# Optimization experiments

Measured on AMD Instinct MI355X. Metric: run time of the kernel, lower is better.

Reference implementation:

```python
import jax, jax.numpy as jnp
import numpy as np

K = 3          # k_neighbors
EPS = 1e-12    # F.normalize eps


def _l2norm(x):
    n = jnp.sqrt(jnp.sum(x * x, axis=-1, keepdims=True))
    return x / jnp.maximum(n, EPS)


def setup_inputs() -> dict:
    key = jax.random.key(0)
    k1, k2 = jax.random.split(key)
    query_features = jax.random.normal(k1, (64, 64, 32, 32), dtype=jnp.float32)
    support_features = jax.random.normal(k2, (64, 5, 64, 1024), dtype=jnp.float32)
    return {"query_features": query_features, "support_features": support_features}


def reference(query_features, support_features):
    B, D, h, w = query_features.shape
    # (B, Nq, D), L2-normalized along D
    q_local = _l2norm(query_features.reshape(B, D, h * w).transpose(0, 2, 1))
    # support: (B, Way, D, Ns) -> (B, Way, Ns, D), L2-normalized along D
    s_local = _l2norm(support_features.transpose(0, 1, 3, 2))
    # cosine similarities for all (batch, way) pairs in one batched matmul
    sim = jnp.einsum('bqd,bwsd->bwqs', q_local, s_local)  # (B, Way, Nq, Ns)
    k_actual = min(K, sim.shape[-1])
    topk_sim, _ = jax.lax.top_k(sim, k_actual)            # (B, Way, Nq, k)
    return topk_sim.sum(axis=(-1, -2))                    # (B, Way)
```

## Files before the change

kernel.cpp:

```cpp
#include <hip/hip_runtime.h>
#include <hip/hip_bf16.h>


using bf16x8 = __attribute__((ext_vector_type(8))) short;
using f32x4  = __attribute__((ext_vector_type(4))) float;

__device__ inline unsigned cvt_pk_bf16(float lo, float hi) {
    unsigned r;
    asm("v_cvt_pk_bf16_f32 %0, %1, %2" : "=v"(r) : "v"(lo), "v"(hi));
    return r;
}

__device__ inline uint4 pack8cvt(const float* v) {
    uint4 r;
    r.x = cvt_pk_bf16(v[0], v[1]);
    r.y = cvt_pk_bf16(v[2], v[3]);
    r.z = cvt_pk_bf16(v[4], v[5]);
    r.w = cvt_pk_bf16(v[6], v[7]);
    return r;
}

#define INS(v, T0, T1, T2) do {                         \
    float _v = (v);                                     \
    float _n0 = fmaxf((T0), _v);                        \
    float _n1 = __builtin_amdgcn_fmed3f(_v, (T0), (T1));\
    float _n2 = __builtin_amdgcn_fmed3f(_v, (T1), (T2));\
    (T0) = _n0; (T1) = _n1; (T2) = _n2;                 \
} while (0)

__global__ void norms_kernel(const float* __restrict__ Q, const float* __restrict__ S,
                             float* __restrict__ rnq, float* __restrict__ rns) {
    int gid = blockIdx.x * blockDim.x + threadIdx.x;
    if (gid < 65536) {
        int b = gid >> 10, qi = gid & 1023;
        const float* p = Q + (size_t)b * 65536 + qi;
        float ss = 0.f;
        #pragma unroll
        for (int d = 0; d < 64; ++d) { float v = p[(size_t)d * 1024]; ss += v * v; }
        rnq[gid] = 1.0f / fmaxf(sqrtf(ss), 1e-12f);
    } else {
        int v = gid - 65536;
        int bw = v >> 10, si = v & 1023;
        const float* p = S + (size_t)bw * 65536 + si;
        float ss = 0.f;
        #pragma unroll
        for (int d = 0; d < 64; ++d) { float x = p[(size_t)d * 1024]; ss += x * x; }
        rns[v] = 1.0f / fmaxf(sqrtf(ss), 1e-12f);
    }
}

__global__ __launch_bounds__(512, 4) void knn_main(
        const float* __restrict__ Q, const float* __restrict__ S,
        const float* __restrict__ rnq, const float* __restrict__ rns,
        float* __restrict__ partial) {
    __shared__ uint4 qfrag[16 * 128];
    __shared__ uint4 sfrag[2][4 * 128];
    __shared__ float wsum[8];

    const int qc = blockIdx.x, w = blockIdx.y, b = blockIdx.z;
    const int t = threadIdx.x, wv = t >> 6, lane = t & 63;

    const float* Qb   = Q + (size_t)b * 65536;
    const float* Sb   = S + (size_t)(b * 5 + w) * 65536;
    const float* rnqb = rnq + (b << 10);
    const float* rnsb = rns + ((b * 5 + w) << 10);

    bf16x8 bq[4][2];
    for (int ph = 0; ph < 2; ++ph) {
        for (int sub = 0; sub < 4; ++sub) {
            int qg = (qc << 9) + (ph << 8) + (sub << 6) + lane;
            float v[8];
            #pragma unroll
            for (int i = 0; i < 8; ++i)
                v[i] = Qb[(size_t)((wv << 3) + i) * 1024 + qg];
            qfrag[((sub << 2) + (lane >> 4)) * 128 + (wv << 4) + (lane & 15)] = pack8cvt(v);
        }
        __syncthreads();
        if ((wv >> 2) == ph) {
            #pragma unroll
            for (int qt = 0; qt < 4; ++qt)
                #pragma unroll
                for (int c = 0; c < 2; ++c)
                    bq[qt][c] = *reinterpret_cast<const bf16x8*>(
                        &qfrag[(((wv & 3) << 2) + qt) * 128 + (c << 6) + lane]);
        }
        __syncthreads();
    }

    {
        float sv[8]; float rs = rnsb[lane];
        #pragma unroll
        for (int i = 0; i < 8; ++i)
            sv[i] = Sb[(size_t)((wv << 3) + i) * 1024 + lane] * rs;
        sfrag[0][(lane >> 4) * 128 + (wv << 4) + (lane & 15)] = pack8cvt(sv);
    }
    __syncthreads();

    float t0[4], t1[4], t2[4];
    #pragma unroll
    for (int qt = 0; qt < 4; ++qt) { t0[qt] = -1e30f; t1[qt] = -1e30f; t2[qt] = -1e30f; }
    int cur = 0;

    const float* sp = Sb + ((wv << 3) << 10) + lane;

    for (int blk = 0; blk < 16; ++blk) {
        float sv[8]; float rs;
        if (blk < 15) {
            const int sb = (blk + 1) << 6;
            rs = rnsb[sb + lane];
            #pragma unroll
            for (int i = 0; i < 8; ++i)
                sv[i] = sp[(size_t)(i << 10) + sb];
        }
        #pragma unroll
        for (int st = 0; st < 4; ++st) {
            bf16x8 a0 = *reinterpret_cast<const bf16x8*>(&sfrag[cur][st * 128 + lane]);
            bf16x8 a1 = *reinterpret_cast<const bf16x8*>(&sfrag[cur][st * 128 + 64 + lane]);
            #pragma unroll
            for (int qt = 0; qt < 4; ++qt) {
                f32x4 c = {0.f, 0.f, 0.f, 0.f};
                c = __builtin_amdgcn_mfma_f32_16x16x32_bf16(a0, bq[qt][0], c, 0, 0, 0);
                c = __builtin_amdgcn_mfma_f32_16x16x32_bf16(a1, bq[qt][1], c, 0, 0, 0);
                #pragma unroll
                for (int j = 0; j < 4; ++j)
                    INS(c[j], t0[qt], t1[qt], t2[qt]);
            }
        }
        if (blk < 15) {
            #pragma unroll
            for (int i = 0; i < 8; ++i) sv[i] *= rs;
            sfrag[cur ^ 1][(lane >> 4) * 128 + (wv << 4) + (lane & 15)] = pack8cvt(sv);
        }
        __syncthreads();
        cur ^= 1;
    }

    float s3 = 0.f;
    #pragma unroll
    for (int qt = 0; qt < 4; ++qt) {
        #pragma unroll
        for (int m = 16; m <= 32; m <<= 1) {
            float b0 = __shfl_xor(t0[qt], m);
            float b1 = __shfl_xor(t1[qt], m);
            float b2 = __shfl_xor(t2[qt], m);
            INS(b0, t0[qt], t1[qt], t2[qt]);
            INS(b1, t0[qt], t1[qt], t2[qt]);
            INS(b2, t0[qt], t1[qt], t2[qt]);
        }
        int qg = (qc << 9) + (wv << 6) + (qt << 4) + (lane & 15);
        s3 += (t0[qt] + t1[qt] + t2[qt]) * rnqb[qg];
    }
    #pragma unroll
    for (int m = 1; m < 64; m <<= 1) s3 += __shfl_xor(s3, m);
    s3 *= 0.25f;
    if (lane == 0) wsum[wv] = s3;
    __syncthreads();
    if (t == 0) {
        float acc = 0.f;
        #pragma unroll
        for (int i = 0; i < 8; ++i) acc += wsum[i];
        partial[((b * 5 + w) << 1) + qc] = acc;
    }
}

__global__ void finalize_kernel(const float* __restrict__ partial, float* __restrict__ out) {
    int i = blockIdx.x * blockDim.x + threadIdx.x;
    if (i < 320)
        out[i] = partial[2 * i] + partial[2 * i + 1];
}

extern "C" void kernel_launch(void* const* d_in, const int* in_sizes, int n_in,
                              void* d_out, int out_size, void* d_ws, size_t ws_size,
                              hipStream_t stream) {
    const float* Q = (const float*)d_in[0];
    const float* S = (const float*)d_in[1];
    float* out = (float*)d_out;

    float* rnq = (float*)d_ws;
    float* rns = rnq + 65536;
    float* partial = rns + 327680;

    norms_kernel<<<(65536 + 327680) / 256, 256, 0, stream>>>(Q, S, rnq, rns);
    dim3 grid(2, 5, 64);
    knn_main<<<grid, 512, 0, stream>>>(Q, S, rnq, rns, partial);
    finalize_kernel<<<2, 256, 0, stream>>>(partial, out);
}
```

Before: 100.0 us.

## Pre-convert Q and S to bf16 MFMA-fragment layout in workspace before KNN

```diff
diff --git a/kernel.cpp b/kernel.cpp
--- a/kernel.cpp
+++ b/kernel.cpp
@@ -28,6 +28,119 @@
     (T0) = _n0; (T1) = _n1; (T2) = _n2;                 \
 } while (0)
 
+
+__global__ __launch_bounds__(256) void prep_q(const float* __restrict__ Q,
+                                              uint4* __restrict__ Qbf,
+                                              float* __restrict__ rnq) {
+    const int b = blockIdx.x >> 2;
+    const int col = ((blockIdx.x & 3) << 8) + threadIdx.x;
+    const float* p = Q + (size_t)b * 65536 + col;
+    float v[64];
+    #pragma unroll
+    for (int d = 0; d < 64; ++d) v[d] = p[(size_t)d << 10];
+    float ss = 0.f;
+    #pragma unroll
+    for (int d = 0; d < 64; ++d) ss += v[d] * v[d];
+    rnq[(b << 10) + col] = 1.0f / fmaxf(sqrtf(ss), 1e-12f);
+    uint4* ob = Qbf + ((size_t)(b << 6) + (col >> 4)) * 128 + (col & 15);
+    #pragma unroll
+    for (int h = 0; h < 8; ++h)
+        ob[h << 4] = pack8cvt(&v[h << 3]);
+}
+
+__global__ __launch_bounds__(256) void prep_s(const float* __restrict__ S,
+                                              uint4* __restrict__ Sbf) {
+    const int bw = blockIdx.x >> 2;
+    const int col = ((blockIdx.x & 3) << 8) + threadIdx.x;
+    const float* p = S + (size_t)bw * 65536 + col;
+    float v[64];
+    #pragma unroll
+    for (int d = 0; d < 64; ++d) v[d] = p[(size_t)d << 10];
+    float ss = 0.f;
+    #pragma unroll
+    for (int d = 0; d < 64; ++d) ss += v[d] * v[d];
+    const float rs = 1.0f / fmaxf(sqrtf(ss), 1e-12f);
+    #pragma unroll
+    for (int d = 0; d < 64; ++d) v[d] *= rs;
+    uint4* ob = Sbf + ((size_t)(bw << 6) + (col >> 4)) * 128 + (col & 15);
+    #pragma unroll
+    for (int h = 0; h < 8; ++h)
+        ob[h << 4] = pack8cvt(&v[h << 3]);
+}
+
+__global__ __launch_bounds__(256) void knn_main(const uint4* __restrict__ Qbf,
+                                                const uint4* __restrict__ Sbf,
+                                                const float* __restrict__ rnq,
+                                                float* __restrict__ partial) {
+    __shared__ float wsum[4];
+    const int qc = blockIdx.x, w = blockIdx.y, b = blockIdx.z;
+    const int wv = threadIdx.x >> 6, lane = threadIdx.x & 63;
+
+    const uint4* qb = Qbf + ((size_t)(b << 6) + (qc << 4) + (wv << 2)) * 128 + lane;
+    bf16x8 bq[4][2];
+    #pragma unroll
+    for (int qt = 0; qt < 4; ++qt)
+        #pragma unroll
+        for (int c = 0; c < 2; ++c)
+            bq[qt][c] = *reinterpret_cast<const bf16x8*>(&qb[qt * 128 + (c << 6)]);
+
+    const uint4* sb = Sbf + (size_t)((b * 5 + w) << 6) * 128 + lane;
+
+    float t0[4], t1[4], t2[4];
+    #pragma unroll
+    for (int qt = 0; qt < 4; ++qt) { t0[qt] = -1e30f; t1[qt] = -1e30f; t2[qt] = -1e30f; }
+
+    bf16x8 a0 = *reinterpret_cast<const bf16x8*>(&sb[0]);
+    bf16x8 a1 = *reinterpret_cast<const bf16x8*>(&sb[64]);
+    #pragma unroll 4
+    for (int st = 0; st < 64; ++st) {
+        const bf16x8 c0 = a0, c1 = a1;
+        if (st < 63) {
+            a0 = *reinterpret_cast<const bf16x8*>(&sb[(st + 1) * 128]);
+            a1 = *reinterpret_cast<const bf16x8*>(&sb[(st + 1) * 128 + 64]);
+        }
+        #pragma unroll
+        for (int qt = 0; qt < 4; ++qt) {
+            f32x4 c = {0.f, 0.f, 0.f, 0.f};
+            c = __builtin_amdgcn_mfma_f32_16x16x32_bf16(c0, bq[qt][0], c, 0, 0, 0);
+            c = __builtin_amdgcn_mfma_f32_16x16x32_bf16(c1, bq[qt][1], c, 0, 0, 0);
+            #pragma unroll
+            for (int j = 0; j < 4; ++j)
+                INS(c[j], t0[qt], t1[qt], t2[qt]);
+        }
+    }
+
+    float s3 = 0.f;
+    #pragma unroll
+    for (int qt = 0; qt < 4; ++qt) {
+        #pragma unroll
+        for (int m = 16; m <= 32; m <<= 1) {
+            float b0 = __shfl_xor(t0[qt], m);
+            float b1 = __shfl_xor(t1[qt], m);
+            float b2 = __shfl_xor(t2[qt], m);
+            INS(b0, t0[qt], t1[qt], t2[qt]);
+            INS(b1, t0[qt], t1[qt], t2[qt]);
+            INS(b2, t0[qt], t1[qt], t2[qt]);
+        }
+        const int qg = (qc << 8) + (wv << 6) + (qt << 4) + (lane & 15);
+        s3 += (t0[qt] + t1[qt] + t2[qt]) * rnq[(b << 10) + qg];
+    }
+    #pragma unroll
+    for (int m = 1; m < 64; m <<= 1) s3 += __shfl_xor(s3, m);
+    s3 *= 0.25f;
+    if (lane == 0) wsum[wv] = s3;
+    __syncthreads();
+    if (threadIdx.x == 0)
+        partial[((b * 5 + w) << 2) + qc] = (wsum[0] + wsum[1]) + (wsum[2] + wsum[3]);
+}
+
+__global__ void finalize4(const float* __restrict__ partial, float* __restrict__ out) {
+    int i = blockIdx.x * blockDim.x + threadIdx.x;
+    if (i < 320)
+        out[i] = (partial[4 * i] + partial[4 * i + 1]) +
+                 (partial[4 * i + 2] + partial[4 * i + 3]);
+}
+
 __global__ void norms_kernel(const float* __restrict__ Q, const float* __restrict__ S,
                              float* __restrict__ rnq, float* __restrict__ rns) {
     int gid = blockIdx.x * blockDim.x + threadIdx.x;
@@ -49,7 +162,7 @@
     }
 }
 
-__global__ __launch_bounds__(512, 4) void knn_main(
+__global__ __launch_bounds__(512, 4) void knn_fb(
         const float* __restrict__ Q, const float* __restrict__ S,
         const float* __restrict__ rnq, const float* __restrict__ rns,
         float* __restrict__ partial) {
@@ -100,17 +213,16 @@
     #pragma unroll
     for (int qt = 0; qt < 4; ++qt) { t0[qt] = -1e30f; t1[qt] = -1e30f; t2[qt] = -1e30f; }
     int cur = 0;
-
     const float* sp = Sb + ((wv << 3) << 10) + lane;
 
     for (int blk = 0; blk < 16; ++blk) {
         float sv[8]; float rs;
         if (blk < 15) {
-            const int sb = (blk + 1) << 6;
-            rs = rnsb[sb + lane];
+            const int sb_ = (blk + 1) << 6;
+            rs = rnsb[sb_ + lane];
             #pragma unroll
             for (int i = 0; i < 8; ++i)
-                sv[i] = sp[(size_t)(i << 10) + sb];
+                sv[i] = sp[(size_t)(i << 10) + sb_];
         }
         #pragma unroll
         for (int st = 0; st < 4; ++st) {
@@ -163,7 +275,7 @@
     }
 }
 
-__global__ void finalize_kernel(const float* __restrict__ partial, float* __restrict__ out) {
+__global__ void finalize2(const float* __restrict__ partial, float* __restrict__ out) {
     int i = blockIdx.x * blockDim.x + threadIdx.x;
     if (i < 320)
         out[i] = partial[2 * i] + partial[2 * i + 1];
@@ -176,12 +288,22 @@
     const float* S = (const float*)d_in[1];
     float* out = (float*)d_out;
 
-    float* rnq = (float*)d_ws;
-    float* rns = rnq + 65536;
-    float* partial = rns + 327680;
-
-    norms_kernel<<<(65536 + 327680) / 256, 256, 0, stream>>>(Q, S, rnq, rns);
-    dim3 grid(2, 5, 64);
-    knn_main<<<grid, 512, 0, stream>>>(Q, S, rnq, rns, partial);
-    finalize_kernel<<<2, 256, 0, stream>>>(partial, out);
-}
+    const size_t NEED = 8388608ull + 41943040ull + 262144ull + 5120ull;
+    if (ws_size >= NEED) {
+        uint4* Qbf    = (uint4*)d_ws;
+        uint4* Sbf    = (uint4*)((char*)d_ws + 8388608ull);
+        float* rnq    = (float*)((char*)d_ws + 8388608ull + 41943040ull);
+        float* partial= (float*)((char*)d_ws + 8388608ull + 41943040ull + 262144ull);
+        prep_q<<<256, 256, 0, stream>>>(Q, Qbf, rnq);
+        prep_s<<<1280, 256, 0, stream>>>(S, Sbf);
+        knn_main<<<dim3(4, 5, 64), 256, 0, stream>>>(Qbf, Sbf, rnq, partial);
+        finalize4<<<2, 256, 0, stream>>>(partial, out);
+    } else {
+        float* rnq = (float*)d_ws;
+        float* rns = rnq + 65536;
+        float* partial = rns + 327680;
+        norms_kernel<<<(65536 + 327680) / 256, 256, 0, stream>>>(Q, S, rnq, rns);
+        knn_fb<<<dim3(2, 5, 64), 512, 0, stream>>>(Q, S, rnq, rns, partial);
+        finalize2<<<2, 256, 0, stream>>>(partial, out);
+    }
+}
```

After: 99.54 us. About the same (-0.5%).
